# Kernel tuning notes

Measured on AMD Instinct MI355X. Metric: run time of the kernel, lower is better.

Reference implementation:

```python
import jax, jax.numpy as jnp
import numpy as np

HEADS = 16


def fenwick_mask(T):
    # Boolean [T, T] mask: diagonal + Fenwick-tree lookback positions, causal.
    m = np.zeros((T, T), dtype=bool)
    for i in range(T):
        j = i + 1
        while j <= T:
            m[i, j - 1] = True
            j += j & -j
        step = 1
        while i - step >= 0:
            m[i, i - step] = True
            step *= 2
    m &= np.tril(np.ones((T, T), dtype=bool))  # causal
    return jnp.asarray(m)


def setup_inputs() -> dict:
    key = jax.random.key(0)
    ks = jax.random.split(key, 4)
    B, T, C = 2, 2048, 1024
    x = jax.random.normal(ks[0], (B, T, C), dtype=jnp.float32)
    W_qkv = jax.random.normal(ks[1], (C, 3 * C), dtype=jnp.float32) * (C ** -0.5)
    b_qkv = jnp.zeros((3 * C,), dtype=jnp.float32)
    W_proj = jax.random.normal(ks[2], (C, C), dtype=jnp.float32) * (C ** -0.5)
    b_proj = jnp.zeros((C,), dtype=jnp.float32)
    return {"x": x, "W_qkv": W_qkv, "b_qkv": b_qkv, "W_proj": W_proj, "b_proj": b_proj}


def reference(x, W_qkv, b_qkv, W_proj, b_proj):
    B, T, C = x.shape
    H = HEADS
    Dh = C // H
    scale = Dh ** -0.5
    qkv = (x @ W_qkv + b_qkv).reshape(B, T, 3, H, Dh)
    qkv = jnp.transpose(qkv, (2, 0, 3, 1, 4))  # [3, B, H, T, Dh]
    q, k, v = qkv[0], qkv[1], qkv[2]
    attn = jnp.einsum('bhtd,bhsd->bhts', q, k) * scale  # [B, H, T, T]
    mask = fenwick_mask(T)  # trace-time constant
    attn = jnp.where(mask[None, None], attn, -jnp.inf)
    attn = jax.nn.softmax(attn, axis=-1)
    out = jnp.einsum('bhts,bhsd->bhtd', attn, v)  # [B, H, T, Dh]
    out = jnp.transpose(out, (0, 2, 1, 3)).reshape(B, T, C)
    return out @ W_proj + b_proj
```

## Files before the change

### kernel.cpp

```cpp
#include <hip/hip_runtime.h>
#include <hip/hip_bf16.h>


typedef unsigned short ushort_t;
typedef __attribute__((ext_vector_type(8))) short s16x8;
typedef __attribute__((ext_vector_type(4))) float f32x4;

#define T_SEQ 2048
#define C_DIM 1024
#define HEADS 16

__device__ __forceinline__ ushort_t f2bf(float f) {
    union { float f; unsigned u; } v{f};
    unsigned r = v.u + 0x7FFFu + ((v.u >> 16) & 1u);
    return (ushort_t)(r >> 16);
}
__device__ __forceinline__ float bf2f(ushort_t u) {
    union { unsigned u; float f; } v{((unsigned)u) << 16};
    return v.f;
}

__device__ __forceinline__ void async16(const ushort_t* g, ushort_t* l) {
    __builtin_amdgcn_global_load_lds(
        (const __attribute__((address_space(1))) void*)g,
        (__attribute__((address_space(3))) void*)l, 16, 0, 0);
}

__global__ void prep(const float* __restrict__ x, ushort_t* __restrict__ xb,
                     const float* __restrict__ Wq, ushort_t* __restrict__ WqT,
                     const float* __restrict__ Wp, ushort_t* __restrict__ WpT) {
    const int bid = blockIdx.x;
    const int tid = threadIdx.x;
    if (bid < 4096) {
        const int i = bid * 256 + tid;
        float4 f = ((const float4*)x)[i];
        ushort4 o;
        o.x = f2bf(f.x); o.y = f2bf(f.y); o.z = f2bf(f.z); o.w = f2bf(f.w);
        ((ushort4*)xb)[i] = o;
    } else {
        __shared__ ushort_t tile[32][33];
        const float* W; ushort_t* WT; int N, nb, kb;
        if (bid < 7168) {
            const int tb = bid - 4096;
            W = Wq; WT = WqT; N = 3072; nb = (tb % 96) * 32; kb = (tb / 96) * 32;
        } else {
            const int tb = bid - 7168;
            W = Wp; WT = WpT; N = 1024; nb = (tb & 31) * 32; kb = (tb >> 5) * 32;
        }
        const int tx = tid & 31, ty = tid >> 5;
        #pragma unroll
        for (int i = ty; i < 32; i += 8)
            tile[i][tx] = f2bf(W[(size_t)(kb + i) * N + nb + tx]);
        __syncthreads();
        #pragma unroll
        for (int i = ty; i < 32; i += 8)
            WT[(size_t)(nb + i) * 1024 + kb + tx] = tile[tx][i];
    }
}

__global__ __launch_bounds__(256, 4)
void gemm_qkv(const ushort_t* __restrict__ A, const ushort_t* __restrict__ BT,
              const float* __restrict__ bias, ushort_t* __restrict__ C,
              int N, int K) {
    __shared__ ushort_t lsA[128 * 64];
    __shared__ ushort_t lsB[128 * 64];

    const int tid  = threadIdx.x;
    const int wave = tid >> 6;
    const int lane = tid & 63;

    const int bid    = blockIdx.x;
    const int xcd    = bid & 7;
    const int q      = bid >> 3;
    const int rowblk = ((xcd & 3) << 3) + (q & 7);
    const int colblk = (xcd >> 2) * 12 + (q >> 3);
    const int row0   = rowblk * 128;
    const int col0   = colblk * 128;

    const int wr   = (wave >> 1) * 64;
    const int wc   = (wave & 1) * 64;
    const int lrow = lane & 15;
    const int quad = lane >> 4;
    const int crow = lane >> 3;
    const int gcol = ((lane & 7) ^ crow) * 8;
    const int d3   = lrow & 7;

    f32x4 acc[4][4] = {};

    for (int k0 = 0; k0 < K; k0 += 64) {
        #pragma unroll
        for (int it = 0; it < 4; ++it) {
            const int chunk = it * 4 + wave;
            const int r = chunk * 8 + crow;
            async16(A  + (size_t)(row0 + r) * K + (k0 + gcol), lsA + chunk * 512);
            async16(BT + (size_t)(col0 + r) * K + (k0 + gcol), lsB + chunk * 512);
        }
        __syncthreads();
        #pragma unroll
        for (int kk = 0; kk < 64; kk += 32) {
            const int g = (kk >> 3) + quad;
            const int slot = (g ^ d3) << 3;
            s16x8 af[4], bfr[4];
            #pragma unroll
            for (int i = 0; i < 4; ++i)
                af[i] = *(const s16x8*)(lsA + (wr + i * 16 + lrow) * 64 + slot);
            #pragma unroll
            for (int j = 0; j < 4; ++j)
                bfr[j] = *(const s16x8*)(lsB + (wc + j * 16 + lrow) * 64 + slot);
            #pragma unroll
            for (int i = 0; i < 4; ++i)
                #pragma unroll
                for (int j = 0; j < 4; ++j)
                    acc[i][j] = __builtin_amdgcn_mfma_f32_16x16x32_bf16(
                        af[i], bfr[j], acc[i][j], 0, 0, 0);
        }
        __syncthreads();
    }

    #pragma unroll
    for (int i = 0; i < 4; ++i) {
        #pragma unroll
        for (int j = 0; j < 4; ++j) {
            const int col = col0 + wc + j * 16 + lrow;
            const float bv = bias[col];
            #pragma unroll
            for (int r = 0; r < 4; ++r) {
                const int row = row0 + wr + i * 16 + quad * 4 + r;
                C[(size_t)row * N + col] = f2bf(acc[i][j][r] + bv);
            }
        }
    }
}

#define PSTAGE(t, b) do {                                                        \
    _Pragma("unroll") for (int it = 0; it < 4; ++it) {                           \
        const int chunk = it * 4 + wave;                                         \
        const int r = chunk * 8 + crow;                                          \
        async16(A  + (size_t)(row0 + r) * K + ((t) * 64 + gcol), lsA[b] + chunk * 512); \
        async16(BT + (size_t)(col0 + r) * K + ((t) * 64 + gcol), lsB[b] + chunk * 512); \
    }                                                                            \
} while (0)

__global__ void gemm_proj(const ushort_t* __restrict__ A, const ushort_t* __restrict__ BT,
                          const float* __restrict__ bias, float* __restrict__ C,
                          int N, int K) {
    __shared__ ushort_t lsA[2][128 * 64];
    __shared__ ushort_t lsB[2][128 * 64];

    const int tid  = threadIdx.x;
    const int wave = tid >> 6;
    const int lane = tid & 63;

    const int bid  = blockIdx.x;
    const int xcd  = bid & 7;
    const int q    = bid >> 3;
    const int row0 = (xcd * 4 + (q & 3)) * 128;
    const int col0 = (q >> 2) * 128;

    const int wr   = (wave >> 1) * 64;
    const int wc   = (wave & 1) * 64;
    const int lrow = lane & 15;
    const int quad = lane >> 4;
    const int crow = lane >> 3;
    const int gcol = ((lane & 7) ^ crow) * 8;
    const int d3   = lrow & 7;

    f32x4 acc[4][4] = {};

    const int nt = K >> 6;
    int cur = 0;
    PSTAGE(0, 0);
    __syncthreads();
    for (int t = 0; t < nt; ++t) {
        if (t + 1 < nt) PSTAGE(t + 1, cur ^ 1);
        #pragma unroll
        for (int kk = 0; kk < 64; kk += 32) {
            const int g = (kk >> 3) + quad;
            const int slot = (g ^ d3) << 3;
            s16x8 af[4], bfr[4];
            #pragma unroll
            for (int i = 0; i < 4; ++i)
                af[i] = *(const s16x8*)(lsA[cur] + (wr + i * 16 + lrow) * 64 + slot);
            #pragma unroll
            for (int j = 0; j < 4; ++j)
                bfr[j] = *(const s16x8*)(lsB[cur] + (wc + j * 16 + lrow) * 64 + slot);
            #pragma unroll
            for (int i = 0; i < 4; ++i)
                #pragma unroll
                for (int j = 0; j < 4; ++j)
                    acc[i][j] = __builtin_amdgcn_mfma_f32_16x16x32_bf16(
                        af[i], bfr[j], acc[i][j], 0, 0, 0);
        }
        __syncthreads();
        cur ^= 1;
    }

    #pragma unroll
    for (int i = 0; i < 4; ++i) {
        #pragma unroll
        for (int j = 0; j < 4; ++j) {
            const int col = col0 + wc + j * 16 + lrow;
            const float bv = bias[col];
            #pragma unroll
            for (int r = 0; r < 4; ++r) {
                const int row = row0 + wr + i * 16 + quad * 4 + r;
                C[(size_t)row * N + col] = acc[i][j][r] + bv;
            }
        }
    }
}

__global__ void fenwick_attn(const ushort_t* __restrict__ QKV, ushort_t* __restrict__ AO) {
    const int lane = threadIdx.x & 63;
    const int bid  = blockIdx.x;
    const int xcd  = bid & 7;
    const int q    = bid >> 3;
    const int bh   = xcd + ((q >> 6) << 3);
    const int tile = ((q & 63) << 2) + (threadIdx.x >> 6);
    const int h    = bh & (HEADS - 1);
    const int b    = bh >> 4;
    const int tl   = lane >> 3;
    const int g    = lane & 7;
    const int t    = tile * 8 + tl;

    const ushort_t* base = QKV + (size_t)(b * T_SEQ) * 3072 + h * 64 + g * 8;

    float qf[8];
    {
        s16x8 qv = *(const s16x8*)(base + (size_t)t * 3072);
        #pragma unroll
        for (int e = 0; e < 8; ++e) qf[e] = bf2f((ushort_t)qv[e]);
    }

    float logit[12];
    int   pos[12];
    float mx = -1e30f;
    #pragma unroll
    for (int s = 0; s < 12; ++s) {
        const int step = (s == 0) ? 0 : (1 << (s - 1));
        const bool act = (step <= t);
        const int p = act ? (t - step) : t;
        pos[s] = p;
        s16x8 kv = *(const s16x8*)(base + (size_t)p * 3072 + 1024);
        float l = 0.f;
        #pragma unroll
        for (int e = 0; e < 8; ++e) l = fmaf(qf[e], bf2f((ushort_t)kv[e]), l);
        l += __shfl_xor(l, 1, 64);
        l += __shfl_xor(l, 2, 64);
        l += __shfl_xor(l, 4, 64);
        l *= 0.125f;
        logit[s] = act ? l : -1e30f;
        mx = fmaxf(mx, logit[s]);
    }

    float denom = 0.f;
    float ov[8] = {};
    #pragma unroll
    for (int s = 0; s < 12; ++s) {
        const float w = __expf(logit[s] - mx);
        denom += w;
        s16x8 vv = *(const s16x8*)(base + (size_t)pos[s] * 3072 + 2048);
        #pragma unroll
        for (int e = 0; e < 8; ++e) ov[e] = fmaf(w, bf2f((ushort_t)vv[e]), ov[e]);
    }

    const float inv = 1.f / denom;
    s16x8 os;
    #pragma unroll
    for (int e = 0; e < 8; ++e) os[e] = (short)f2bf(ov[e] * inv);
    *(s16x8*)(AO + (size_t)(b * T_SEQ + t) * C_DIM + h * 64 + g * 8) = os;
}

extern "C" void kernel_launch(void* const* d_in, const int* in_sizes, int n_in,
                              void* d_out, int out_size, void* d_ws, size_t ws_size,
                              hipStream_t stream) {
    const float* x      = (const float*)d_in[0];
    const float* W_qkv  = (const float*)d_in[1];
    const float* b_qkv  = (const float*)d_in[2];
    const float* W_proj = (const float*)d_in[3];
    const float* b_proj = (const float*)d_in[4];
    float* out = (float*)d_out;

    char* ws = (char*)d_ws;
    ushort_t* xb     = (ushort_t*)(ws);
    ushort_t* WqkvT  = (ushort_t*)(ws + (size_t)8  * 1048576);
    ushort_t* QKVb   = (ushort_t*)(ws + (size_t)14 * 1048576);
    ushort_t* AO     = (ushort_t*)(ws + (size_t)38 * 1048576);
    ushort_t* WprojT = (ushort_t*)(ws + (size_t)46 * 1048576);

    prep<<<8192, 256, 0, stream>>>(x, xb, W_qkv, WqkvT, W_proj, WprojT);
    gemm_qkv<<<768, 256, 0, stream>>>(xb, WqkvT, b_qkv, QKVb, 3072, 1024);
    fenwick_attn<<<2048, 256, 0, stream>>>(QKVb, AO);
    gemm_proj<<<256, 256, 0, stream>>>(AO, WprojT, b_proj, out, 1024, 1024);
}
```

Baseline: 149.4 us.

## Enlarge QKV GEMM tiles to 256x192 with double-buffered async LDS loads

The QKV projection GEMM now uses 256x192 output tiles per block instead of 128x128, so the grid drops from 768 to 256 blocks, about one per CU. Each wave holds a 128x96 accumulator. Global-to-LDS loads are double-buffered so the next K-slice is fetched while the current one feeds the MFMAs. This raises operand reuse and cuts barrier stalls per MFMA, but uses much more LDS and registers (launch bounds dropped to 1 block per CU) and leaves less parallel slack to hide latency.

```diff
diff --git a/kernel.cpp b/kernel.cpp
--- a/kernel.cpp
+++ b/kernel.cpp
@@ -58,78 +58,91 @@
     }
 }
 
-__global__ __launch_bounds__(256, 4)
+__global__ __launch_bounds__(256, 1)
 void gemm_qkv(const ushort_t* __restrict__ A, const ushort_t* __restrict__ BT,
               const float* __restrict__ bias, ushort_t* __restrict__ C,
               int N, int K) {
-    __shared__ ushort_t lsA[128 * 64];
-    __shared__ ushort_t lsB[128 * 64];
+    __shared__ ushort_t lds[2][28672];
 
     const int tid  = threadIdx.x;
     const int wave = tid >> 6;
     const int lane = tid & 63;
+    const int wm   = wave >> 1;
+    const int wn   = wave & 1;
+    const int lrow = lane & 15;
+    const int quad = lane >> 4;
+    const int d3   = lrow & 7;
+    const int crow = lane >> 3;
+    const int gcol = (((lane & 7) ^ crow) << 3);
 
     const int bid    = blockIdx.x;
     const int xcd    = bid & 7;
     const int q      = bid >> 3;
-    const int rowblk = ((xcd & 3) << 3) + (q & 7);
-    const int colblk = (xcd >> 2) * 12 + (q >> 3);
-    const int row0   = rowblk * 128;
-    const int col0   = colblk * 128;
-
-    const int wr   = (wave >> 1) * 64;
-    const int wc   = (wave & 1) * 64;
-    const int lrow = lane & 15;
-    const int quad = lane >> 4;
-    const int crow = lane >> 3;
-    const int gcol = ((lane & 7) ^ crow) * 8;
-    const int d3   = lrow & 7;
-
-    f32x4 acc[4][4] = {};
-
-    for (int k0 = 0; k0 < K; k0 += 64) {
-        #pragma unroll
-        for (int it = 0; it < 4; ++it) {
-            const int chunk = it * 4 + wave;
-            const int r = chunk * 8 + crow;
-            async16(A  + (size_t)(row0 + r) * K + (k0 + gcol), lsA + chunk * 512);
-            async16(BT + (size_t)(col0 + r) * K + (k0 + gcol), lsB + chunk * 512);
-        }
+    const int rowblk = ((xcd & 3) << 2) + (q & 3);
+    const int colblk = ((xcd >> 2) << 3) + (q >> 2);
+    const int row0   = rowblk * 256;
+    const int col0   = colblk * 192;
+
+    const ushort_t* Ag = A  + (size_t)(row0 + wave * 8 + crow) * K + gcol;
+    const ushort_t* Bg = BT + (size_t)(col0 + wave * 8 + crow) * K + gcol;
+
+    f32x4 acc[8][6] = {};
+
+    #define QSTAGE(t, b) do {                                                      \
+        _Pragma("unroll") for (int u = 0; u < 8; ++u)                              \
+            async16(Ag + (size_t)(u) * 32 * K + (size_t)(t) * 64,                  \
+                    &lds[b][u * 2048 + wave * 512]);                               \
+        _Pragma("unroll") for (int u = 0; u < 6; ++u)                              \
+            async16(Bg + (size_t)(u) * 32 * K + (size_t)(t) * 64,                  \
+                    &lds[b][16384 + u * 2048 + wave * 512]);                       \
+    } while (0)
+
+    const int nt = K >> 6;
+    int cur = 0;
+    QSTAGE(0, 0);
+    __syncthreads();
+
+    for (int t = 0; t < nt; ++t) {
+        if (t + 1 < nt) QSTAGE(t + 1, cur ^ 1);
+        s16x8 af[8][2], bfr[6][2];
+        #pragma unroll
+        for (int i = 0; i < 8; ++i)
+            #pragma unroll
+            for (int kh = 0; kh < 2; ++kh)
+                af[i][kh] = *(const s16x8*)(&lds[cur][
+                    ((wm << 7) + i * 16 + lrow) * 64 + (((kh * 4 + quad) ^ d3) << 3)]);
+        #pragma unroll
+        for (int j = 0; j < 6; ++j)
+            #pragma unroll
+            for (int kh = 0; kh < 2; ++kh)
+                bfr[j][kh] = *(const s16x8*)(&lds[cur][16384 +
+                    (wn * 96 + j * 16 + lrow) * 64 + (((kh * 4 + quad) ^ d3) << 3)]);
+        #pragma unroll
+        for (int i = 0; i < 8; ++i)
+            #pragma unroll
+            for (int j = 0; j < 6; ++j)
+                #pragma unroll
+                for (int kh = 0; kh < 2; ++kh)
+                    acc[i][j] = __builtin_amdgcn_mfma_f32_16x16x32_bf16(
+                        af[i][kh], bfr[j][kh], acc[i][j], 0, 0, 0);
         __syncthreads();
-        #pragma unroll
-        for (int kk = 0; kk < 64; kk += 32) {
-            const int g = (kk >> 3) + quad;
-            const int slot = (g ^ d3) << 3;
-            s16x8 af[4], bfr[4];
-            #pragma unroll
-            for (int i = 0; i < 4; ++i)
-                af[i] = *(const s16x8*)(lsA + (wr + i * 16 + lrow) * 64 + slot);
-            #pragma unroll
-            for (int j = 0; j < 4; ++j)
-                bfr[j] = *(const s16x8*)(lsB + (wc + j * 16 + lrow) * 64 + slot);
-            #pragma unroll
-            for (int i = 0; i < 4; ++i)
-                #pragma unroll
-                for (int j = 0; j < 4; ++j)
-                    acc[i][j] = __builtin_amdgcn_mfma_f32_16x16x32_bf16(
-                        af[i], bfr[j], acc[i][j], 0, 0, 0);
-        }
-        __syncthreads();
-    }
-
-    #pragma unroll
-    for (int i = 0; i < 4; ++i) {
-        #pragma unroll
-        for (int j = 0; j < 4; ++j) {
-            const int col = col0 + wc + j * 16 + lrow;
+        cur ^= 1;
+    }
+
+    #pragma unroll
+    for (int i = 0; i < 8; ++i) {
+        #pragma unroll
+        for (int j = 0; j < 6; ++j) {
+            const int col = col0 + wn * 96 + j * 16 + lrow;
             const float bv = bias[col];
             #pragma unroll
             for (int r = 0; r < 4; ++r) {
-                const int row = row0 + wr + i * 16 + quad * 4 + r;
+                const int row = row0 + (wm << 7) + i * 16 + quad * 4 + r;
                 C[(size_t)row * N + col] = f2bf(acc[i][j][r] + bv);
             }
         }
     }
+    #undef QSTAGE
 }
 
 #define PSTAGE(t, b) do {                                                        \
@@ -289,7 +302,7 @@
     ushort_t* WprojT = (ushort_t*)(ws + (size_t)46 * 1048576);
 
     prep<<<8192, 256, 0, stream>>>(x, xb, W_qkv, WqkvT, W_proj, WprojT);
-    gemm_qkv<<<768, 256, 0, stream>>>(xb, WqkvT, b_qkv, QKVb, 3072, 1024);
+    gemm_qkv<<<256, 256, 0, stream>>>(xb, WqkvT, b_qkv, QKVb, 3072, 1024);
     fenwick_attn<<<2048, 256, 0, stream>>>(QKVb, AO);
     gemm_proj<<<256, 256, 0, stream>>>(AO, WprojT, b_proj, out, 1024, 1024);
 }
```

Result: no change. 149.1 us (-0.2%).
